# Performance work log

Hardware: AMD Instinct MI355X
Metric: run time of the kernel (lower is better)

Reference implementation:

```python
import jax, jax.numpy as jnp
import numpy as np


def _decode(fm):
    # fm: [B, A, H, W, 5+C] YOLO head output
    B, A, H, W, D = fm.shape
    box = fm[..., :4].reshape(B, -1, 4)
    conf = jax.nn.sigmoid(fm[..., 4].reshape(B, -1))
    cls = jax.nn.sigmoid(fm[..., 5:].reshape(B, -1, D - 5))
    # Faithful to the torch in-place sequence:
    #   b0 = (b0 - b2/2)*W ; b1 = (b1 - b3/2)*H
    #   b2 = (NEW b0 + OLD b2/2)*W ; b3 = (NEW b1 + OLD b3/2)*H
    w = jnp.asarray(W, fm.dtype)
    h = jnp.asarray(H, fm.dtype)
    x1 = (box[..., 0] - box[..., 2] / 2) * w
    y1 = (box[..., 1] - box[..., 3] / 2) * h
    x2 = (x1 + box[..., 2] / 2) * w
    y2 = (y1 + box[..., 3] / 2) * h
    boxes = jnp.stack([x1, y1, x2, y2], axis=-1)  # [B, A*H*W, 4]
    return boxes, conf, cls


def setup_inputs() -> dict:
    key = jax.random.key(0)
    k0, k1, k2, k3 = jax.random.split(key, 4)
    B, A, C = 16, 3, 80
    fm0 = jax.random.uniform(k0, (B, A, 80, 80, 5 + C), dtype=jnp.float32)
    fm1 = jax.random.uniform(k1, (B, A, 40, 40, 5 + C), dtype=jnp.float32)
    fm2 = jax.random.uniform(k2, (B, A, 20, 20, 5 + C), dtype=jnp.float32)
    detection_targets = jax.random.uniform(k3, (1, 4), dtype=jnp.float32)
    return {"fm0": fm0, "fm1": fm1, "fm2": fm2,
            "detection_targets": detection_targets}


def reference(fm0, fm1, fm2, detection_targets):
    boxes, scores, classes = [], [], []
    for fm in (fm0, fm1, fm2):
        b, s, c = _decode(fm)
        boxes.append(b)
        scores.append(s)
        classes.append(c)
    all_boxes = jnp.concatenate(boxes, axis=1)    # [B, N, 4]
    all_scores = jnp.concatenate(scores, axis=1)  # [B, N]
    all_classes = jnp.concatenate(classes, axis=1)  # [B, N, C]
    # Pack like the torch nms_input: [x1, y1, x2, y2, conf, cls...]
    return jnp.concatenate(
        [all_boxes, all_scores[..., None], all_classes], axis=-1)  # [B, N, 5+C]
```

## Files before the change

### kernel.cpp

```cpp
#include <hip/hip_runtime.h>

#define NROWS_OUT 25200
#define L0_FLOATS 26112000
#define L1_FLOATS 6528000
#define L2_FLOATS 1632000
#define TOTAL_FLOATS (L0_FLOATS + L1_FLOATS + L2_FLOATS)
#define TOTAL4   (TOTAL_FLOATS / 4)
#define HALF4    (TOTAL4 / 2)

typedef float v4f __attribute__((ext_vector_type(4)));

__device__ __forceinline__ float fast_sigmoid(float x) {
    float e = __expf(-x);
    return __builtin_amdgcn_rcpf(1.0f + e);
}

template <int ROWS, int OFF, int SCALE>
__device__ __forceinline__ void process4(const float* __restrict__ in,
                                         float* __restrict__ out,
                                         int f_local) {
    constexpr int ROWS85 = ROWS * 85;
    const int b   = f_local / ROWS85;
    const int rem = f_local - b * ROWS85;
    const int c0  = rem % 85;

    int g = f_local;
    if (c0 <= 3)  g = f_local - c0;
    if (c0 >= 82) g = f_local + (85 - c0);

    const v4f x = *(const v4f*)(in + f_local);
    const float r0 = in[g + 0];
    const float r1 = in[g + 1];
    const float r2 = in[g + 2];
    const float r3 = in[g + 3];

    const float sc = (float)SCALE;
    const float h2 = 0.5f * r2, h3 = 0.5f * r3;
    const float q0 = (r0 - h2) * sc;
    const float q1 = (r1 - h3) * sc;
    const float q2 = (q0 + h2) * sc;
    const float q3 = (q1 + h3) * sc;

    float xv[4] = {x.x, x.y, x.z, x.w};
    float y[4];
#pragma unroll
    for (int k = 0; k < 4; ++k) {
        int c = c0 + k;
        if (c >= 85) c -= 85;
        const float s = fast_sigmoid(xv[k]);
        const float q = (c == 0) ? q0 : ((c == 1) ? q1 : ((c == 2) ? q2 : q3));
        y[k] = (c < 4) ? q : s;
    }

    const int out_f = (b * NROWS_OUT + OFF) * 85 + rem;
    v4f yo; yo.x = y[0]; yo.y = y[1]; yo.z = y[2]; yo.w = y[3];
    __builtin_nontemporal_store(yo, (v4f*)(out + out_f));
}

__device__ __forceinline__ void dispatch4(const float* __restrict__ fm0,
                                          const float* __restrict__ fm1,
                                          const float* __restrict__ fm2,
                                          float* __restrict__ out, int f) {
    if (f < L0_FLOATS) {
        process4<19200, 0, 80>(fm0, out, f);
    } else if (f < L0_FLOATS + L1_FLOATS) {
        process4<4800, 19200, 40>(fm1, out, f - L0_FLOATS);
    } else {
        process4<1200, 24000, 20>(fm2, out, f - (L0_FLOATS + L1_FLOATS));
    }
}

__global__ __launch_bounds__(256) void yolo_decode_kernel(
    const float* __restrict__ fm0, const float* __restrict__ fm1,
    const float* __restrict__ fm2, float* __restrict__ out) {
    const int v = blockIdx.x * 256 + threadIdx.x;
    if (v >= HALF4) return;
    dispatch4(fm0, fm1, fm2, out, v * 4);
    dispatch4(fm0, fm1, fm2, out, (v + HALF4) * 4);
}

extern "C" void kernel_launch(void* const* d_in, const int* in_sizes, int n_in,
                              void* d_out, int out_size, void* d_ws, size_t ws_size,
                              hipStream_t stream) {
    const float* fm0 = (const float*)d_in[0];
    const float* fm1 = (const float*)d_in[1];
    const float* fm2 = (const float*)d_in[2];
    float* out = (float*)d_out;

    const int blocks = (HALF4 + 255) / 256;
    hipLaunchKernelGGL(yolo_decode_kernel, dim3(blocks), dim3(256), 0, stream,
                       fm0, fm1, fm2, out);
}
```

Measured before the change: 237.0 us.

## Stage input tiles in LDS with halos and split blocks per pyramid level

Each block now loads a contiguous 512-vector tile of one feature map into shared memory, plus one halo vector on each side. The box coordinates each thread needs are read from LDS instead of with four extra scalar global loads. Blocks are assigned to pyramid levels by block index, so the per-element level branch is gone and each block works on contiguous data. This costs a __syncthreads per block and some LDS traffic. The earlier scalar reloads probably hit cache already, so the savings may be small.

```diff
diff --git a/kernel.cpp b/kernel.cpp
--- a/kernel.cpp
+++ b/kernel.cpp
@@ -1,38 +1,36 @@
 #include <hip/hip_runtime.h>
 
 #define NROWS_OUT 25200
-#define L0_FLOATS 26112000
-#define L1_FLOATS 6528000
-#define L2_FLOATS 1632000
-#define TOTAL_FLOATS (L0_FLOATS + L1_FLOATS + L2_FLOATS)
-#define TOTAL4   (TOTAL_FLOATS / 4)
-#define HALF4    (TOTAL4 / 2)
+
+#define L0_BLOCKS 12750
+#define L1_BLOCKS 3188
+#define L2_BLOCKS 797
+#define TOTAL_BLOCKS (L0_BLOCKS + L1_BLOCKS + L2_BLOCKS)
 
 typedef float v4f __attribute__((ext_vector_type(4)));
 
 __device__ __forceinline__ float fast_sigmoid(float x) {
-    float e = __expf(-x);
-    return __builtin_amdgcn_rcpf(1.0f + e);
+    return __builtin_amdgcn_rcpf(1.0f + __expf(-x));
 }
 
 template <int ROWS, int OFF, int SCALE>
-__device__ __forceinline__ void process4(const float* __restrict__ in,
-                                         float* __restrict__ out,
-                                         int f_local) {
+__device__ __forceinline__ void emit4(float* __restrict__ out,
+                                      const float* __restrict__ ldsf,
+                                      int basef, int v, v4f x) {
+    const int f = v * 4;
     constexpr int ROWS85 = ROWS * 85;
-    const int b   = f_local / ROWS85;
-    const int rem = f_local - b * ROWS85;
+    const int b   = f / ROWS85;
+    const int rem = f - b * ROWS85;
     const int c0  = rem % 85;
 
-    int g = f_local;
-    if (c0 <= 3)  g = f_local - c0;
-    if (c0 >= 82) g = f_local + (85 - c0);
-
-    const v4f x = *(const v4f*)(in + f_local);
-    const float r0 = in[g + 0];
-    const float r1 = in[g + 1];
-    const float r2 = in[g + 2];
-    const float r3 = in[g + 3];
+    int g = f;
+    if (c0 <= 3)  g = f - c0;
+    if (c0 >= 82) g = f + (85 - c0);
+    const int lo = g - basef + 4;
+    const float r0 = ldsf[lo + 0];
+    const float r1 = ldsf[lo + 1];
+    const float r2 = ldsf[lo + 2];
+    const float r3 = ldsf[lo + 3];
 
     const float sc = (float)SCALE;
     const float h2 = 0.5f * r2, h3 = 0.5f * r3;
@@ -57,26 +55,50 @@
     __builtin_nontemporal_store(yo, (v4f*)(out + out_f));
 }
 
-__device__ __forceinline__ void dispatch4(const float* __restrict__ fm0,
-                                          const float* __restrict__ fm1,
-                                          const float* __restrict__ fm2,
-                                          float* __restrict__ out, int f) {
-    if (f < L0_FLOATS) {
-        process4<19200, 0, 80>(fm0, out, f);
-    } else if (f < L0_FLOATS + L1_FLOATS) {
-        process4<4800, 19200, 40>(fm1, out, f - L0_FLOATS);
-    } else {
-        process4<1200, 24000, 20>(fm2, out, f - (L0_FLOATS + L1_FLOATS));
+template <int ROWS, int OFF, int SCALE, int NF4>
+__device__ __forceinline__ void run_level(const float* __restrict__ in,
+                                          float* __restrict__ out,
+                                          v4f* __restrict__ lds4, int bb) {
+    const int t     = threadIdx.x;
+    const int base4 = bb * 512;
+    const int basef = base4 * 4;
+
+    const int v1 = base4 + t;
+    const int v2 = base4 + 256 + t;
+    const bool a1 = v1 < NF4;
+    const bool a2 = v2 < NF4;
+
+    v4f x1, x2;
+    if (a1) { x1 = *(const v4f*)(in + v1 * 4); lds4[1 + t]   = x1; }
+    if (a2) { x2 = *(const v4f*)(in + v2 * 4); lds4[257 + t] = x2; }
+    if (t == 0) {
+        int hv = base4 - 1; if (hv < 0) hv = 0;
+        lds4[0] = *(const v4f*)(in + hv * 4);
     }
+    if (t == 255) {
+        int hv = base4 + 512; if (hv > NF4 - 1) hv = NF4 - 1;
+        lds4[513] = *(const v4f*)(in + hv * 4);
+    }
+    __syncthreads();
+
+    const float* ldsf = (const float*)lds4;
+    if (a1) emit4<ROWS, OFF, SCALE>(out, ldsf, basef, v1, x1);
+    if (a2) emit4<ROWS, OFF, SCALE>(out, ldsf, basef, v2, x2);
 }
 
 __global__ __launch_bounds__(256) void yolo_decode_kernel(
     const float* __restrict__ fm0, const float* __restrict__ fm1,
     const float* __restrict__ fm2, float* __restrict__ out) {
-    const int v = blockIdx.x * 256 + threadIdx.x;
-    if (v >= HALF4) return;
-    dispatch4(fm0, fm1, fm2, out, v * 4);
-    dispatch4(fm0, fm1, fm2, out, (v + HALF4) * 4);
+    __shared__ v4f lds4[514];
+    const int bb = blockIdx.x;
+    if (bb < L0_BLOCKS) {
+        run_level<19200, 0, 80, 6528000>(fm0, out, lds4, bb);
+    } else if (bb < L0_BLOCKS + L1_BLOCKS) {
+        run_level<4800, 19200, 40, 1632000>(fm1, out, lds4, bb - L0_BLOCKS);
+    } else {
+        run_level<1200, 24000, 20, 408000>(fm2, out, lds4,
+                                           bb - (L0_BLOCKS + L1_BLOCKS));
+    }
 }
 
 extern "C" void kernel_launch(void* const* d_in, const int* in_sizes, int n_in,
@@ -87,7 +109,6 @@
     const float* fm2 = (const float*)d_in[2];
     float* out = (float*)d_out;
 
-    const int blocks = (HALF4 + 255) / 256;
-    hipLaunchKernelGGL(yolo_decode_kernel, dim3(blocks), dim3(256), 0, stream,
-                       fm0, fm1, fm2, out);
+    hipLaunchKernelGGL(yolo_decode_kernel, dim3(TOTAL_BLOCKS), dim3(256), 0,
+                       stream, fm0, fm1, fm2, out);
 }
```

Result: no change. 237.9 us (+0.4%).
